# Kernel optimization log

Hardware: AMD Instinct MI355X
Metric: run time of the kernel (lower is better)

Reference implementation:

```python
import jax, jax.numpy as jnp
import numpy as np

DIM = 256
HEADS = 8
WS = 8
N = WS * WS  # 64 tokens per window


def _rel_pos_index(ws: int) -> np.ndarray:
    coords = np.arange(ws)
    grid = np.stack(np.meshgrid(coords, coords, indexing='ij')).reshape(2, -1)  # [2, ws^2]
    rel = grid[:, :, None] - grid[:, None, :]          # [2, N, N]
    rel = rel.transpose(1, 2, 0).copy()                # [N, N, 2]
    rel[:, :, 0] += ws - 1
    rel[:, :, 1] += ws - 1
    rel[:, :, 0] *= 2 * ws - 1
    return rel.sum(-1)                                 # [N, N] int

REL_IDX = jnp.asarray(_rel_pos_index(WS))


def setup_inputs() -> dict:
    key = jax.random.key(0)
    ks = jax.random.split(key, 9)
    B = 4096
    std = 0.02
    return {
        'query_tokens': jax.random.normal(ks[0], (B, N, DIM), jnp.float32),
        'source_tokens': jax.random.normal(ks[1], (B, N, DIM), jnp.float32),
        'Wq': jax.random.normal(ks[2], (DIM, DIM), jnp.float32) * std,
        'bq': jnp.zeros((DIM,), jnp.float32),
        'Wkv': jax.random.normal(ks[3], (DIM, 2 * DIM), jnp.float32) * std,
        'bkv': jnp.zeros((2 * DIM,), jnp.float32),
        'bias_table': jax.random.normal(ks[4], ((2 * WS - 1) ** 2, HEADS), jnp.float32) * std,
        'Wp': jax.random.normal(ks[5], (DIM, DIM), jnp.float32) * std,
        'bp': jnp.zeros((DIM,), jnp.float32),
    }


def reference(query_tokens, source_tokens, Wq, bq, Wkv, bkv, bias_table, Wp, bp):
    B_, n, C = query_tokens.shape
    d = C // HEADS
    scale = d ** -0.5
    # projections
    q = (query_tokens @ Wq + bq).reshape(B_, n, HEADS, d).transpose(0, 2, 1, 3) * scale  # [B,H,N,d]
    kv = (source_tokens @ Wkv + bkv).reshape(B_, n, 2, HEADS, d).transpose(2, 0, 3, 1, 4)
    k, v = kv[0], kv[1]                                    # [B,H,N,d]
    # attention with relative position bias
    attn = jnp.einsum('bhnd,bhmd->bhnm', q, k)             # [B,H,N,N]
    rel_bias = bias_table[REL_IDX]                         # [N,N,H]
    attn = attn + rel_bias.transpose(2, 0, 1)[None]        # + [1,H,N,N]
    attn = jax.nn.softmax(attn, axis=-1)
    out = jnp.einsum('bhnm,bhmd->bhnd', attn, v)           # [B,H,N,d]
    out = out.transpose(0, 2, 1, 3).reshape(B_, n, C)
    return out @ Wp + bp
```

## Files before the change

### kernel.cpp

```cpp
#include <hip/hip_runtime.h>

typedef __bf16 bf16;
typedef __bf16 bf16x8 __attribute__((ext_vector_type(8)));
typedef __bf16 bf16x4 __attribute__((ext_vector_type(4)));
typedef float  f32x4  __attribute__((ext_vector_type(4)));

#define LDA   264
#define LDV   72
#define LDP   72
#define OFF_K (64 * LDA)
#define OFF_V (128 * LDA)
#define OFF_P (128 * LDA + 256 * LDV)
#define LDS_ELEMS (OFF_P + 8 * 32 * LDP)

static __device__ __forceinline__ f32x4 mfma16(bf16x8 a, bf16x8 b, f32x4 c) {
  return __builtin_amdgcn_mfma_f32_16x16x32_bf16(a, b, c, 0, 0, 0);
}

__global__ void prep_kernel(const float* __restrict__ Wq, const float* __restrict__ Wkv,
                            const float* __restrict__ Wp, const float* __restrict__ btab,
                            bf16* __restrict__ WqT, bf16* __restrict__ WkvT,
                            bf16* __restrict__ WpT, float* __restrict__ biasT) {
  int idx = blockIdx.x * 512 + threadIdx.x;
  if (idx < 65536) {
    int n = idx >> 8, k = idx & 255;
    WqT[idx] = (bf16)Wq[k * 256 + n];
  } else if (idx < 196608) {
    int j = idx - 65536, n = j >> 8, k = j & 255;
    WkvT[j] = (bf16)Wkv[k * 512 + n];
  } else if (idx < 262144) {
    int j = idx - 196608, n = j >> 8, k = j & 255;
    WpT[j] = (bf16)Wp[k * 256 + n];
  } else {
    int j = idx - 262144;
    int h = j >> 12, ck = (j >> 6) & 63, rq = j & 63;
    int rel = ((rq >> 3) - (ck >> 3) + 7) * 15 + ((rq & 7) - (ck & 7) + 7);
    biasT[j] = btab[rel * 8 + h];
  }
}

__global__ __launch_bounds__(512, 2) void fused_kernel(
    const float* __restrict__ Xq_g, const float* __restrict__ Xs_g,
    const float* __restrict__ bq,  const float* __restrict__ bkv,
    const float* __restrict__ bp,
    const bf16* __restrict__ WqT, const bf16* __restrict__ WkvT,
    const bf16* __restrict__ WpT, const float* __restrict__ biasT,
    float* __restrict__ out) {
  __shared__ __attribute__((aligned(16))) bf16 sm[LDS_ELEMS];
  const int tid  = (int)threadIdx.x;
  const int w    = tid >> 6;
  const int lane = tid & 63;
  const int c    = lane & 15;
  const int q    = lane >> 4;
  bf16* A_ = sm;
  bf16* K_ = sm + OFF_K;
  bf16* V_ = sm + OFF_V;
  bf16* P_ = sm + OFF_P + w * (32 * LDP);
  const long long xoff = (long long)blockIdx.x * (64 * 256);

  {
    const float4* src = (const float4*)(Xs_g + xoff);
    #pragma unroll
    for (int i = 0; i < 8; ++i) {
      int chunk = tid + i * 512;
      int row = chunk >> 6, col = (chunk & 63) << 2;
      float4 v = src[chunk];
      bf16x4 b4 = {(bf16)v.x, (bf16)v.y, (bf16)v.z, (bf16)v.w};
      *(bf16x4*)(A_ + row * LDA + col) = b4;
    }
  }
  __syncthreads();

  {
    f32x4 acc[4][4];
    #pragma unroll
    for (int nt = 0; nt < 4; ++nt) {
      float bv = bkv[w * 64 + nt * 16 + c];
      #pragma unroll
      for (int mt = 0; mt < 4; ++mt) acc[mt][nt] = (f32x4){bv, bv, bv, bv};
    }
    #pragma unroll
    for (int kt = 0; kt < 8; ++kt) {
      bf16x8 af[4], bw[4];
      #pragma unroll
      for (int mt = 0; mt < 4; ++mt)
        af[mt] = *(const bf16x8*)(A_ + (mt * 16 + c) * LDA + kt * 32 + q * 8);
      #pragma unroll
      for (int nt = 0; nt < 4; ++nt)
        bw[nt] = *(const bf16x8*)(WkvT + (w * 64 + nt * 16 + c) * 256 + kt * 32 + q * 8);
      #pragma unroll
      for (int mt = 0; mt < 4; ++mt)
        #pragma unroll
        for (int nt = 0; nt < 4; ++nt)
          acc[mt][nt] = mfma16(af[mt], bw[nt], acc[mt][nt]);
    }
    if (w < 4) {
      #pragma unroll
      for (int mt = 0; mt < 4; ++mt)
        #pragma unroll
        for (int nt = 0; nt < 4; ++nt)
          #pragma unroll
          for (int r = 0; r < 4; ++r)
            K_[(mt * 16 + q * 4 + r) * LDA + w * 64 + nt * 16 + c] = (bf16)acc[mt][nt][r];
    } else {
      #pragma unroll
      for (int mt = 0; mt < 4; ++mt)
        #pragma unroll
        for (int nt = 0; nt < 4; ++nt)
          #pragma unroll
          for (int r = 0; r < 4; ++r)
            V_[((w - 4) * 64 + nt * 16 + c) * LDV + mt * 16 + q * 4 + r] = (bf16)acc[mt][nt][r];
    }
  }
  __syncthreads();

  {
    const float4* src = (const float4*)(Xq_g + xoff);
    #pragma unroll
    for (int i = 0; i < 8; ++i) {
      int chunk = tid + i * 512;
      int row = chunk >> 6, col = (chunk & 63) << 2;
      float4 v = src[chunk];
      bf16x4 b4 = {(bf16)v.x, (bf16)v.y, (bf16)v.z, (bf16)v.w};
      *(bf16x4*)(A_ + row * LDA + col) = b4;
    }
  }
  __syncthreads();

  f32x4 qacc[4][2];
  {
    #pragma unroll
    for (int nt = 0; nt < 2; ++nt) {
      float bv = bq[w * 32 + nt * 16 + c];
      #pragma unroll
      for (int mt = 0; mt < 4; ++mt) qacc[mt][nt] = (f32x4){bv, bv, bv, bv};
    }
    #pragma unroll
    for (int kt = 0; kt < 8; ++kt) {
      bf16x8 af[4], bw[2];
      #pragma unroll
      for (int mt = 0; mt < 4; ++mt)
        af[mt] = *(const bf16x8*)(A_ + (mt * 16 + c) * LDA + kt * 32 + q * 8);
      #pragma unroll
      for (int nt = 0; nt < 2; ++nt)
        bw[nt] = *(const bf16x8*)(WqT + (w * 32 + nt * 16 + c) * 256 + kt * 32 + q * 8);
      #pragma unroll
      for (int mt = 0; mt < 4; ++mt)
        #pragma unroll
        for (int nt = 0; nt < 2; ++nt)
          qacc[mt][nt] = mfma16(af[mt], bw[nt], qacc[mt][nt]);
    }
  }
  __syncthreads();
  {
    const float scale = 0.17677669529663687f;
    #pragma unroll
    for (int mt = 0; mt < 4; ++mt)
      #pragma unroll
      for (int nt = 0; nt < 2; ++nt)
        #pragma unroll
        for (int r = 0; r < 4; ++r)
          A_[(mt * 16 + q * 4 + r) * LDA + w * 32 + nt * 16 + c] = (bf16)(qacc[mt][nt][r] * scale);
  }

  bf16x8 aq[4];
  #pragma unroll
  for (int mt = 0; mt < 4; ++mt)
    aq[mt] = *(const bf16x8*)(A_ + (mt * 16 + c) * LDA + w * 32 + q * 8);

  #pragma unroll
  for (int p = 0; p < 2; ++p) {
    f32x4 s[2][4];
    #pragma unroll
    for (int mt = 0; mt < 2; ++mt)
      #pragma unroll
      for (int nt = 0; nt < 4; ++nt)
        s[mt][nt] = *(const f32x4*)(biasT + (w * 64 + nt * 16 + c) * 64 + p * 32 + mt * 16 + q * 4);
    bf16x8 bk[4];
    #pragma unroll
    for (int nt = 0; nt < 4; ++nt)
      bk[nt] = *(const bf16x8*)(K_ + (nt * 16 + c) * LDA + w * 32 + q * 8);
    #pragma unroll
    for (int mt = 0; mt < 2; ++mt)
      #pragma unroll
      for (int nt = 0; nt < 4; ++nt)
        s[mt][nt] = mfma16(aq[p * 2 + mt], bk[nt], s[mt][nt]);

    float rl[2][4];
    #pragma unroll
    for (int mt = 0; mt < 2; ++mt) {
      #pragma unroll
      for (int r = 0; r < 4; ++r) {
        float m0 = fmaxf(fmaxf(s[mt][0][r], s[mt][1][r]), fmaxf(s[mt][2][r], s[mt][3][r]));
        m0 = fmaxf(m0, __shfl_xor(m0, 1));
        m0 = fmaxf(m0, __shfl_xor(m0, 2));
        m0 = fmaxf(m0, __shfl_xor(m0, 4));
        m0 = fmaxf(m0, __shfl_xor(m0, 8));
        const float L2E = 1.4426950408889634f;
        float t0 = exp2f((s[mt][0][r] - m0) * L2E);
        float t1 = exp2f((s[mt][1][r] - m0) * L2E);
        float t2 = exp2f((s[mt][2][r] - m0) * L2E);
        float t3 = exp2f((s[mt][3][r] - m0) * L2E);
        s[mt][0][r] = t0; s[mt][1][r] = t1; s[mt][2][r] = t2; s[mt][3][r] = t3;
        float sum = (t0 + t1) + (t2 + t3);
        sum += __shfl_xor(sum, 1);
        sum += __shfl_xor(sum, 2);
        sum += __shfl_xor(sum, 4);
        sum += __shfl_xor(sum, 8);
        rl[mt][r] = __builtin_amdgcn_rcpf(sum);
      }
    }
    #pragma unroll
    for (int mt = 0; mt < 2; ++mt)
      #pragma unroll
      for (int nt = 0; nt < 4; ++nt)
        #pragma unroll
        for (int r = 0; r < 4; ++r)
          P_[(mt * 16 + q * 4 + r) * LDP + nt * 16 + c] = (bf16)s[mt][nt][r];

    bf16x8 bv2[2][2];
    #pragma unroll
    for (int nt = 0; nt < 2; ++nt)
      #pragma unroll
      for (int t = 0; t < 2; ++t)
        bv2[nt][t] = *(const bf16x8*)(V_ + (w * 32 + nt * 16 + c) * LDV + t * 32 + q * 8);
    #pragma unroll
    for (int mt = 0; mt < 2; ++mt) {
      bf16x8 ap0 = *(const bf16x8*)(P_ + (mt * 16 + c) * LDP + q * 8);
      bf16x8 ap1 = *(const bf16x8*)(P_ + (mt * 16 + c) * LDP + 32 + q * 8);
      #pragma unroll
      for (int nt = 0; nt < 2; ++nt) {
        f32x4 o = (f32x4){0.f, 0.f, 0.f, 0.f};
        o = mfma16(ap0, bv2[nt][0], o);
        o = mfma16(ap1, bv2[nt][1], o);
        #pragma unroll
        for (int r = 0; r < 4; ++r)
          A_[(p * 32 + mt * 16 + q * 4 + r) * LDA + w * 32 + nt * 16 + c] =
              (bf16)(o[r] * rl[mt][r]);
      }
    }
  }
  __syncthreads();

  {
    f32x4 acc[4][2];
    #pragma unroll
    for (int nt = 0; nt < 2; ++nt) {
      float bv = bp[w * 32 + nt * 16 + c];
      #pragma unroll
      for (int mt = 0; mt < 4; ++mt) acc[mt][nt] = (f32x4){bv, bv, bv, bv};
    }
    #pragma unroll
    for (int kt = 0; kt < 8; ++kt) {
      bf16x8 af[4], bw[2];
      #pragma unroll
      for (int mt = 0; mt < 4; ++mt)
        af[mt] = *(const bf16x8*)(A_ + (mt * 16 + c) * LDA + kt * 32 + q * 8);
      #pragma unroll
      for (int nt = 0; nt < 2; ++nt)
        bw[nt] = *(const bf16x8*)(WpT + (w * 32 + nt * 16 + c) * 256 + kt * 32 + q * 8);
      #pragma unroll
      for (int mt = 0; mt < 4; ++mt)
        #pragma unroll
        for (int nt = 0; nt < 2; ++nt)
          acc[mt][nt] = mfma16(af[mt], bw[nt], acc[mt][nt]);
    }
    float* dst = out + xoff;
    #pragma unroll
    for (int mt = 0; mt < 4; ++mt)
      #pragma unroll
      for (int nt = 0; nt < 2; ++nt)
        #pragma unroll
        for (int r = 0; r < 4; ++r)
          dst[(mt * 16 + q * 4 + r) * 256 + w * 32 + nt * 16 + c] = acc[mt][nt][r];
  }
}

extern "C" void kernel_launch(void* const* d_in, const int* in_sizes, int n_in,
                              void* d_out, int out_size, void* d_ws, size_t ws_size,
                              hipStream_t stream) {
  const float* Xq   = (const float*)d_in[0];
  const float* Xs   = (const float*)d_in[1];
  const float* Wq   = (const float*)d_in[2];
  const float* bq   = (const float*)d_in[3];
  const float* Wkv  = (const float*)d_in[4];
  const float* bkv  = (const float*)d_in[5];
  const float* btab = (const float*)d_in[6];
  const float* Wp   = (const float*)d_in[7];
  const float* bp   = (const float*)d_in[8];
  float* out = (float*)d_out;

  char* ws = (char*)d_ws;
  bf16*  WqT   = (bf16*)(ws);
  bf16*  WkvT  = (bf16*)(ws + 131072);
  bf16*  WpT   = (bf16*)(ws + 393216);
  float* biasT = (float*)(ws + 524288);

  const int Bw = in_sizes[0] / (64 * 256);

  prep_kernel<<<dim3(576), dim3(512), 0, stream>>>(Wq, Wkv, Wp, btab,
                                                   WqT, WkvT, WpT, biasT);
  fused_kernel<<<dim3(Bw), dim3(512), 0, stream>>>(Xq, Xs, bq, bkv, bp,
                                                   WqT, WkvT, WpT, biasT, out);
}
```

Measured before the change: 924.4 us.

## Keep K/V/Q in registers via lane shuffles, shrink LDS, raise occupancy

Each wave now computes the K and V projections only for its own head, using transposed MFMA operand order. It redistributes the accumulators into MFMA operand layout with cross-lane shuffles instead of round-tripping K, V, Q and P through shared memory. Both input tiles are loaded up front, the softmax scale is folded into WqT during prep, and the bias table is transposed to match. LDS use drops to two 64x264 bf16 buffers, so launch bounds rise to 4 blocks per CU. The cost is more shuffle instructions and higher register pressure under the tighter launch bound.

After: 842.7 us. 8.8% less time.

```diff
diff --git a/kernel.cpp b/kernel.cpp
--- a/kernel.cpp
+++ b/kernel.cpp
@@ -5,16 +5,36 @@
 typedef __bf16 bf16x4 __attribute__((ext_vector_type(4)));
 typedef float  f32x4  __attribute__((ext_vector_type(4)));
 
-#define LDA   264
-#define LDV   72
-#define LDP   72
-#define OFF_K (64 * LDA)
-#define OFF_V (128 * LDA)
-#define OFF_P (128 * LDA + 256 * LDV)
-#define LDS_ELEMS (OFF_P + 8 * 32 * LDP)
+#define LDA 264
+#define LDS_ELEMS (2 * 64 * LDA)
 
 static __device__ __forceinline__ f32x4 mfma16(bf16x8 a, bf16x8 b, f32x4 c) {
   return __builtin_amdgcn_mfma_f32_16x16x32_bf16(a, b, c, 0, 0, 0);
+}
+
+static __device__ __forceinline__ unsigned pk2(float x, float y) {
+  union { bf16 h; unsigned short u; } a, b;
+  a.h = (bf16)x; b.h = (bf16)y;
+  return (unsigned)a.u | ((unsigned)b.u << 16);
+}
+
+static __device__ __forceinline__ bf16x8 redist(f32x4 t0, f32x4 t1,
+                                                int srcA, bool hi) {
+  unsigned p0 = pk2(t0[0], t0[1]);
+  unsigned p1 = pk2(t0[2], t0[3]);
+  unsigned p2 = pk2(t1[0], t1[1]);
+  unsigned p3 = pk2(t1[2], t1[3]);
+  int srcB = srcA + 16;
+  unsigned a0 = __shfl(p0, srcA), a1 = __shfl(p1, srcA);
+  unsigned a2 = __shfl(p2, srcA), a3 = __shfl(p3, srcA);
+  unsigned b0 = __shfl(p0, srcB), b1 = __shfl(p1, srcB);
+  unsigned b2 = __shfl(p2, srcB), b3 = __shfl(p3, srcB);
+  union { unsigned u[4]; bf16x8 v; } r;
+  r.u[0] = hi ? a2 : a0;
+  r.u[1] = hi ? a3 : a1;
+  r.u[2] = hi ? b2 : b0;
+  r.u[3] = hi ? b3 : b1;
+  return r.v;
 }
 
 __global__ void prep_kernel(const float* __restrict__ Wq, const float* __restrict__ Wkv,
@@ -24,7 +44,7 @@
   int idx = blockIdx.x * 512 + threadIdx.x;
   if (idx < 65536) {
     int n = idx >> 8, k = idx & 255;
-    WqT[idx] = (bf16)Wq[k * 256 + n];
+    WqT[idx] = (bf16)(Wq[k * 256 + n] * 0.17677669529663687f);
   } else if (idx < 196608) {
     int j = idx - 65536, n = j >> 8, k = j & 255;
     WkvT[j] = (bf16)Wkv[k * 512 + n];
@@ -33,13 +53,13 @@
     WpT[j] = (bf16)Wp[k * 256 + n];
   } else {
     int j = idx - 262144;
-    int h = j >> 12, ck = (j >> 6) & 63, rq = j & 63;
+    int h = j >> 12, rq = (j >> 6) & 63, ck = j & 63;
     int rel = ((rq >> 3) - (ck >> 3) + 7) * 15 + ((rq & 7) - (ck & 7) + 7);
     biasT[j] = btab[rel * 8 + h];
   }
 }
 
-__global__ __launch_bounds__(512, 2) void fused_kernel(
+__global__ __launch_bounds__(512, 4) void fused_kernel(
     const float* __restrict__ Xq_g, const float* __restrict__ Xs_g,
     const float* __restrict__ bq,  const float* __restrict__ bkv,
     const float* __restrict__ bp,
@@ -52,227 +72,205 @@
   const int lane = tid & 63;
   const int c    = lane & 15;
   const int q    = lane >> 4;
-  bf16* A_ = sm;
-  bf16* K_ = sm + OFF_K;
-  bf16* V_ = sm + OFF_V;
-  bf16* P_ = sm + OFF_P + w * (32 * LDP);
+  const int srcA = c + ((q & 1) << 5);
+  const bool hi  = (q >> 1) != 0;
+  bf16* X0 = sm;
+  bf16* X1 = sm + 64 * LDA;
   const long long xoff = (long long)blockIdx.x * (64 * 256);
 
   {
-    const float4* src = (const float4*)(Xs_g + xoff);
+    const float4* g0 = (const float4*)(Xs_g + xoff);
+    const float4* g1 = (const float4*)(Xq_g + xoff);
+    float4 v0[8], v1[8];
+    #pragma unroll
+    for (int i = 0; i < 8; ++i) v0[i] = g0[tid + i * 512];
+    #pragma unroll
+    for (int i = 0; i < 8; ++i) v1[i] = g1[tid + i * 512];
     #pragma unroll
     for (int i = 0; i < 8; ++i) {
       int chunk = tid + i * 512;
       int row = chunk >> 6, col = (chunk & 63) << 2;
-      float4 v = src[chunk];
-      bf16x4 b4 = {(bf16)v.x, (bf16)v.y, (bf16)v.z, (bf16)v.w};
-      *(bf16x4*)(A_ + row * LDA + col) = b4;
+      bf16x4 s0 = {(bf16)v0[i].x, (bf16)v0[i].y, (bf16)v0[i].z, (bf16)v0[i].w};
+      bf16x4 s1 = {(bf16)v1[i].x, (bf16)v1[i].y, (bf16)v1[i].z, (bf16)v1[i].w};
+      *(bf16x4*)(X0 + row * LDA + col) = s0;
+      *(bf16x4*)(X1 + row * LDA + col) = s1;
     }
   }
   __syncthreads();
 
+  bf16x8 ka[4];
+  bf16x8 vb[2][2];
+  bf16x8 qb[4];
+
   {
-    f32x4 acc[4][4];
-    #pragma unroll
-    for (int nt = 0; nt < 4; ++nt) {
-      float bv = bkv[w * 64 + nt * 16 + c];
-      #pragma unroll
-      for (int mt = 0; mt < 4; ++mt) acc[mt][nt] = (f32x4){bv, bv, bv, bv};
+    f32x4 ak[2][4];
+    f32x4 av[4][2];
+    #pragma unroll
+    for (int m = 0; m < 2; ++m) {
+      f32x4 b4 = *(const f32x4*)(bkv + w * 32 + m * 16 + q * 4);
+      #pragma unroll
+      for (int n = 0; n < 4; ++n) ak[m][n] = b4;
+    }
+    #pragma unroll
+    for (int n = 0; n < 2; ++n) {
+      float bv = bkv[256 + w * 32 + n * 16 + c];
+      #pragma unroll
+      for (int m = 0; m < 4; ++m) av[m][n] = (f32x4){bv, bv, bv, bv};
     }
     #pragma unroll
     for (int kt = 0; kt < 8; ++kt) {
-      bf16x8 af[4], bw[4];
-      #pragma unroll
-      for (int mt = 0; mt < 4; ++mt)
-        af[mt] = *(const bf16x8*)(A_ + (mt * 16 + c) * LDA + kt * 32 + q * 8);
-      #pragma unroll
-      for (int nt = 0; nt < 4; ++nt)
-        bw[nt] = *(const bf16x8*)(WkvT + (w * 64 + nt * 16 + c) * 256 + kt * 32 + q * 8);
-      #pragma unroll
-      for (int mt = 0; mt < 4; ++mt)
-        #pragma unroll
-        for (int nt = 0; nt < 4; ++nt)
-          acc[mt][nt] = mfma16(af[mt], bw[nt], acc[mt][nt]);
-    }
-    if (w < 4) {
-      #pragma unroll
-      for (int mt = 0; mt < 4; ++mt)
-        #pragma unroll
-        for (int nt = 0; nt < 4; ++nt)
-          #pragma unroll
-          for (int r = 0; r < 4; ++r)
-            K_[(mt * 16 + q * 4 + r) * LDA + w * 64 + nt * 16 + c] = (bf16)acc[mt][nt][r];
-    } else {
-      #pragma unroll
-      for (int mt = 0; mt < 4; ++mt)
-        #pragma unroll
-        for (int nt = 0; nt < 4; ++nt)
-          #pragma unroll
-          for (int r = 0; r < 4; ++r)
-            V_[((w - 4) * 64 + nt * 16 + c) * LDV + mt * 16 + q * 4 + r] = (bf16)acc[mt][nt][r];
-    }
+      bf16x8 xf[4], wk[2], wv[2];
+      #pragma unroll
+      for (int m = 0; m < 4; ++m)
+        xf[m] = *(const bf16x8*)(X0 + (m * 16 + c) * LDA + kt * 32 + q * 8);
+      #pragma unroll
+      for (int m = 0; m < 2; ++m)
+        wk[m] = *(const bf16x8*)(WkvT + (w * 32 + m * 16 + c) * 256 + kt * 32 + q * 8);
+      #pragma unroll
+      for (int n = 0; n < 2; ++n)
+        wv[n] = *(const bf16x8*)(WkvT + (256 + w * 32 + n * 16 + c) * 256 + kt * 32 + q * 8);
+      #pragma unroll
+      for (int m = 0; m < 2; ++m)
+        #pragma unroll
+        for (int n = 0; n < 4; ++n)
+          ak[m][n] = mfma16(wk[m], xf[n], ak[m][n]);
+      #pragma unroll
+      for (int m = 0; m < 4; ++m)
+        #pragma unroll
+        for (int n = 0; n < 2; ++n)
+          av[m][n] = mfma16(xf[m], wv[n], av[m][n]);
+    }
+    #pragma unroll
+    for (int t = 0; t < 4; ++t) ka[t] = redist(ak[0][t], ak[1][t], srcA, hi);
+    #pragma unroll
+    for (int n = 0; n < 2; ++n)
+      #pragma unroll
+      for (int t = 0; t < 2; ++t)
+        vb[n][t] = redist(av[2 * t][n], av[2 * t + 1][n], srcA, hi);
+  }
+
+  {
+    const float scale = 0.17677669529663687f;
+    f32x4 aq[2][4];
+    #pragma unroll
+    for (int m = 0; m < 2; ++m) {
+      f32x4 b4 = *(const f32x4*)(bq + w * 32 + m * 16 + q * 4);
+      f32x4 s4 = {b4[0] * scale, b4[1] * scale, b4[2] * scale, b4[3] * scale};
+      #pragma unroll
+      for (int n = 0; n < 4; ++n) aq[m][n] = s4;
+    }
+    #pragma unroll
+    for (int kt = 0; kt < 8; ++kt) {
+      bf16x8 xf[4], wq[2];
+      #pragma unroll
+      for (int m = 0; m < 4; ++m)
+        xf[m] = *(const bf16x8*)(X1 + (m * 16 + c) * LDA + kt * 32 + q * 8);
+      #pragma unroll
+      for (int m = 0; m < 2; ++m)
+        wq[m] = *(const bf16x8*)(WqT + (w * 32 + m * 16 + c) * 256 + kt * 32 + q * 8);
+      #pragma unroll
+      for (int m = 0; m < 2; ++m)
+        #pragma unroll
+        for (int n = 0; n < 4; ++n)
+          aq[m][n] = mfma16(wq[m], xf[n], aq[m][n]);
+    }
+    #pragma unroll
+    for (int t = 0; t < 4; ++t) qb[t] = redist(aq[0][t], aq[1][t], srcA, hi);
   }
   __syncthreads();
 
+  #pragma unroll
+  for (int p = 0; p < 2; ++p) {
+    f32x4 s[4][2];
+    #pragma unroll
+    for (int m = 0; m < 4; ++m)
+      #pragma unroll
+      for (int n = 0; n < 2; ++n)
+        s[m][n] = *(const f32x4*)(biasT + w * 4096 +
+                                  (p * 32 + n * 16 + c) * 64 + m * 16 + q * 4);
+    #pragma unroll
+    for (int m = 0; m < 4; ++m)
+      #pragma unroll
+      for (int n = 0; n < 2; ++n)
+        s[m][n] = mfma16(ka[m], qb[p * 2 + n], s[m][n]);
+
+    #pragma unroll
+    for (int n = 0; n < 2; ++n) {
+      float mx = s[0][n][0];
+      #pragma unroll
+      for (int m = 0; m < 4; ++m)
+        #pragma unroll
+        for (int r = 0; r < 4; ++r) mx = fmaxf(mx, s[m][n][r]);
+      mx = fmaxf(mx, __shfl_xor(mx, 16));
+      mx = fmaxf(mx, __shfl_xor(mx, 32));
+      const float L2E = 1.4426950408889634f;
+      float mb = mx * L2E;
+      float sum = 0.f;
+      #pragma unroll
+      for (int m = 0; m < 4; ++m)
+        #pragma unroll
+        for (int r = 0; r < 4; ++r) {
+          float t = exp2f(s[m][n][r] * L2E - mb);
+          s[m][n][r] = t;
+          sum += t;
+        }
+      sum += __shfl_xor(sum, 16);
+      sum += __shfl_xor(sum, 32);
+      float rl = __builtin_amdgcn_rcpf(sum);
+      #pragma unroll
+      for (int m = 0; m < 4; ++m)
+        #pragma unroll
+        for (int r = 0; r < 4; ++r) s[m][n][r] *= rl;
+    }
+
+    #pragma unroll
+    for (int n = 0; n < 2; ++n) {
+      bf16x8 pa0 = redist(s[0][n], s[1][n], srcA, hi);
+      bf16x8 pa1 = redist(s[2][n], s[3][n], srcA, hi);
+      #pragma unroll
+      for (int d = 0; d < 2; ++d) {
+        f32x4 o = (f32x4){0.f, 0.f, 0.f, 0.f};
+        o = mfma16(pa0, vb[d][0], o);
+        o = mfma16(pa1, vb[d][1], o);
+        #pragma unroll
+        for (int r = 0; r < 4; ++r)
+          X0[(p * 32 + n * 16 + q * 4 + r) * LDA + w * 32 + d * 16 + c] = (bf16)o[r];
+      }
+    }
+  }
+  __syncthreads();
+
   {
-    const float4* src = (const float4*)(Xq_g + xoff);
-    #pragma unroll
-    for (int i = 0; i < 8; ++i) {
-      int chunk = tid + i * 512;
-      int row = chunk >> 6, col = (chunk & 63) << 2;
-      float4 v = src[chunk];
-      bf16x4 b4 = {(bf16)v.x, (bf16)v.y, (bf16)v.z, (bf16)v.w};
-      *(bf16x4*)(A_ + row * LDA + col) = b4;
-    }
-  }
-  __syncthreads();
-
-  f32x4 qacc[4][2];
-  {
-    #pragma unroll
-    for (int nt = 0; nt < 2; ++nt) {
-      float bv = bq[w * 32 + nt * 16 + c];
-      #pragma unroll
-      for (int mt = 0; mt < 4; ++mt) qacc[mt][nt] = (f32x4){bv, bv, bv, bv};
+    f32x4 acc[4][2];
+    #pragma unroll
+    for (int n = 0; n < 2; ++n) {
+      float bv = bp[w * 32 + n * 16 + c];
+      #pragma unroll
+      for (int m = 0; m < 4; ++m) acc[m][n] = (f32x4){bv, bv, bv, bv};
     }
     #pragma unroll
     for (int kt = 0; kt < 8; ++kt) {
       bf16x8 af[4], bw[2];
       #pragma unroll
-      for (int mt = 0; mt < 4; ++mt)
-        af[mt] = *(const bf16x8*)(A_ + (mt * 16 + c) * LDA + kt * 32 + q * 8);
-      #pragma unroll
-      for (int nt = 0; nt < 2; ++nt)
-        bw[nt] = *(const bf16x8*)(WqT + (w * 32 + nt * 16 + c) * 256 + kt * 32 + q * 8);
-      #pragma unroll
-      for (int mt = 0; mt < 4; ++mt)
-        #pragma unroll
-        for (int nt = 0; nt < 2; ++nt)
-          qacc[mt][nt] = mfma16(af[mt], bw[nt], qacc[mt][nt]);
-    }
-  }
-  __syncthreads();
-  {
-    const float scale = 0.17677669529663687f;
-    #pragma unroll
-    for (int mt = 0; mt < 4; ++mt)
-      #pragma unroll
-      for (int nt = 0; nt < 2; ++nt)
+      for (int m = 0; m < 4; ++m)
+        af[m] = *(const bf16x8*)(X0 + (m * 16 + c) * LDA + kt * 32 + q * 8);
+      #pragma unroll
+      for (int n = 0; n < 2; ++n)
+        bw[n] = *(const bf16x8*)(WpT + (w * 32 + n * 16 + c) * 256 + kt * 32 + q * 8);
+      #pragma unroll
+      for (int m = 0; m < 4; ++m)
+        #pragma unroll
+        for (int n = 0; n < 2; ++n)
+          acc[m][n] = mfma16(af[m], bw[n], acc[m][n]);
+    }
+    float* dst = out + xoff;
+    #pragma unroll
+    for (int m = 0; m < 4; ++m)
+      #pragma unroll
+      for (int n = 0; n < 2; ++n)
         #pragma unroll
         for (int r = 0; r < 4; ++r)
-          A_[(mt * 16 + q * 4 + r) * LDA + w * 32 + nt * 16 + c] = (bf16)(qacc[mt][nt][r] * scale);
-  }
-
-  bf16x8 aq[4];
-  #pragma unroll
-  for (int mt = 0; mt < 4; ++mt)
-    aq[mt] = *(const bf16x8*)(A_ + (mt * 16 + c) * LDA + w * 32 + q * 8);
-
-  #pragma unroll
-  for (int p = 0; p < 2; ++p) {
-    f32x4 s[2][4];
-    #pragma unroll
-    for (int mt = 0; mt < 2; ++mt)
-      #pragma unroll
-      for (int nt = 0; nt < 4; ++nt)
-        s[mt][nt] = *(const f32x4*)(biasT + (w * 64 + nt * 16 + c) * 64 + p * 32 + mt * 16 + q * 4);
-    bf16x8 bk[4];
-    #pragma unroll
-    for (int nt = 0; nt < 4; ++nt)
-      bk[nt] = *(const bf16x8*)(K_ + (nt * 16 + c) * LDA + w * 32 + q * 8);
-    #pragma unroll
-    for (int mt = 0; mt < 2; ++mt)
-      #pragma unroll
-      for (int nt = 0; nt < 4; ++nt)
-        s[mt][nt] = mfma16(aq[p * 2 + mt], bk[nt], s[mt][nt]);
-
-    float rl[2][4];
-    #pragma unroll
-    for (int mt = 0; mt < 2; ++mt) {
-      #pragma unroll
-      for (int r = 0; r < 4; ++r) {
-        float m0 = fmaxf(fmaxf(s[mt][0][r], s[mt][1][r]), fmaxf(s[mt][2][r], s[mt][3][r]));
-        m0 = fmaxf(m0, __shfl_xor(m0, 1));
-        m0 = fmaxf(m0, __shfl_xor(m0, 2));
-        m0 = fmaxf(m0, __shfl_xor(m0, 4));
-        m0 = fmaxf(m0, __shfl_xor(m0, 8));
-        const float L2E = 1.4426950408889634f;
-        float t0 = exp2f((s[mt][0][r] - m0) * L2E);
-        float t1 = exp2f((s[mt][1][r] - m0) * L2E);
-        float t2 = exp2f((s[mt][2][r] - m0) * L2E);
-        float t3 = exp2f((s[mt][3][r] - m0) * L2E);
-        s[mt][0][r] = t0; s[mt][1][r] = t1; s[mt][2][r] = t2; s[mt][3][r] = t3;
-        float sum = (t0 + t1) + (t2 + t3);
-        sum += __shfl_xor(sum, 1);
-        sum += __shfl_xor(sum, 2);
-        sum += __shfl_xor(sum, 4);
-        sum += __shfl_xor(sum, 8);
-        rl[mt][r] = __builtin_amdgcn_rcpf(sum);
-      }
-    }
-    #pragma unroll
-    for (int mt = 0; mt < 2; ++mt)
-      #pragma unroll
-      for (int nt = 0; nt < 4; ++nt)
-        #pragma unroll
-        for (int r = 0; r < 4; ++r)
-          P_[(mt * 16 + q * 4 + r) * LDP + nt * 16 + c] = (bf16)s[mt][nt][r];
-
-    bf16x8 bv2[2][2];
-    #pragma unroll
-    for (int nt = 0; nt < 2; ++nt)
-      #pragma unroll
-      for (int t = 0; t < 2; ++t)
-        bv2[nt][t] = *(const bf16x8*)(V_ + (w * 32 + nt * 16 + c) * LDV + t * 32 + q * 8);
-    #pragma unroll
-    for (int mt = 0; mt < 2; ++mt) {
-      bf16x8 ap0 = *(const bf16x8*)(P_ + (mt * 16 + c) * LDP + q * 8);
-      bf16x8 ap1 = *(const bf16x8*)(P_ + (mt * 16 + c) * LDP + 32 + q * 8);
-      #pragma unroll
-      for (int nt = 0; nt < 2; ++nt) {
-        f32x4 o = (f32x4){0.f, 0.f, 0.f, 0.f};
-        o = mfma16(ap0, bv2[nt][0], o);
-        o = mfma16(ap1, bv2[nt][1], o);
-        #pragma unroll
-        for (int r = 0; r < 4; ++r)
-          A_[(p * 32 + mt * 16 + q * 4 + r) * LDA + w * 32 + nt * 16 + c] =
-              (bf16)(o[r] * rl[mt][r]);
-      }
-    }
-  }
-  __syncthreads();
-
-  {
-    f32x4 acc[4][2];
-    #pragma unroll
-    for (int nt = 0; nt < 2; ++nt) {
-      float bv = bp[w * 32 + nt * 16 + c];
-      #pragma unroll
-      for (int mt = 0; mt < 4; ++mt) acc[mt][nt] = (f32x4){bv, bv, bv, bv};
-    }
-    #pragma unroll
-    for (int kt = 0; kt < 8; ++kt) {
-      bf16x8 af[4], bw[2];
-      #pragma unroll
-      for (int mt = 0; mt < 4; ++mt)
-        af[mt] = *(const bf16x8*)(A_ + (mt * 16 + c) * LDA + kt * 32 + q * 8);
-      #pragma unroll
-      for (int nt = 0; nt < 2; ++nt)
-        bw[nt] = *(const bf16x8*)(WpT + (w * 32 + nt * 16 + c) * 256 + kt * 32 + q * 8);
-      #pragma unroll
-      for (int mt = 0; mt < 4; ++mt)
-        #pragma unroll
-        for (int nt = 0; nt < 2; ++nt)
-          acc[mt][nt] = mfma16(af[mt], bw[nt], acc[mt][nt]);
-    }
-    float* dst = out + xoff;
-    #pragma unroll
-    for (int mt = 0; mt < 4; ++mt)
-      #pragma unroll
-      for (int nt = 0; nt < 2; ++nt)
-        #pragma unroll
-        for (int r = 0; r < 4; ++r)
-          dst[(mt * 16 + q * 4 + r) * 256 + w * 32 + nt * 16 + c] = acc[mt][nt][r];
+          dst[(m * 16 + q * 4 + r) * 256 + w * 32 + n * 16 + c] = acc[m][n][r];
   }
 }
 
```
